# Kernel optimization log

Hardware: AMD Instinct MI355X
Metric: run time of the kernel (lower is better)

## Reference

```python
import jax, jax.numpy as jnp
import numpy as np

EPS = 1e-5  # BatchNorm eps (torch default)
K = 16      # num_neighbors


def _bn(x, gamma, beta, axes):
    # training-mode BatchNorm (biased variance), channel axis = 1
    mu = x.mean(axes, keepdims=True)
    var = x.var(axes, keepdims=True)
    shp = [1] * x.ndim
    shp[1] = -1
    return (x - mu) * jax.lax.rsqrt(var + EPS) * gamma.reshape(shp) + beta.reshape(shp)


def setup_inputs() -> dict:
    key = jax.random.key(0)
    ks = jax.random.split(key, 6)
    B, C, N, E = 4, 3, 4096, 256
    s = lambda k_, shp, fan: jax.random.normal(k_, shp, jnp.float32) * np.float32(1.0 / np.sqrt(fan))
    return {
        "x": jax.random.normal(ks[0], (B, C, N), jnp.float32),
        "g1": jnp.ones((C,), jnp.float32), "b1": jnp.zeros((C,), jnp.float32),
        "W1": s(ks[1], (E, C), C), "bw1": jnp.zeros((E,), jnp.float32),
        "g2a": jnp.ones((C,), jnp.float32), "b2a": jnp.zeros((C,), jnp.float32),
        "W2a": s(ks[2], (E, C), C),
        "g2b": jnp.ones((E,), jnp.float32), "b2b": jnp.zeros((E,), jnp.float32),
        "W2b": s(ks[3], (E, E), E),
        "Wf": s(ks[4], (E, 2 * E), 2 * E), "bf": jnp.zeros((E,), jnp.float32),
    }


def reference(x, g1, b1, W1, bw1, g2a, b2a, W2a, g2b, b2b, W2b, Wf, bf):
    B, C, N = x.shape
    xn = _bn(x, g1, b1, (0, 2))                               # BatchNorm1d
    point_emb = jnp.einsum('ec,bcn->ben', W1, xn) + bw1[None, :, None]  # conv1 (1x1)
    # dist = -||xi - xj||; torch topk(dist, largest=False) picks the K LARGEST
    # distances. Squared distance is monotone in the norm, so top_k on d2 gives
    # identical indices without materializing [B,3,N,N].
    x2 = jnp.sum(xn * xn, axis=1)                             # [B,N]
    d2 = x2[:, :, None] + x2[:, None, :] - 2.0 * jnp.einsum('bcn,bcm->bnm', xn, xn)
    _, idx = jax.lax.top_k(d2, min(K, N))                     # [B,N,K]
    idx = idx[:, :, 1:]                                       # original loop skips index 0
    gathered = jax.vmap(lambda xb, ib: xb[:, ib])(xn, idx)    # [B,C,N,K-1]
    neigh = gathered - xn[:, :, :, None]                      # edge features
    h = _bn(neigh, g2a, b2a, (0, 2, 3))                       # BatchNorm2d(Cin)
    h = jnp.einsum('ec,bcnk->benk', W2a, h)                   # 1x1 conv, no bias
    h = jax.nn.gelu(_bn(h, g2b, b2b, (0, 2, 3)), approximate=False)
    h = jnp.einsum('fe,benk->bfnk', W2b, h)                   # 1x1 conv, no bias
    neigh_emb = h.max(-1)                                     # max over neighbors
    feat = jnp.concatenate([point_emb, neigh_emb], axis=1)    # [B,2E,N]
    return jnp.einsum('of,bfn->bon', Wf, feat) + bf[None, :, None]
```

## Files before the change

kernel.cpp:

```cpp
#include <hip/hip_runtime.h>
#include <float.h>
#include <math.h>

#define EPS 1e-5f
constexpr int B = 4, C = 3, N = 4096, E = 256;
constexpr int KNN = 15;
constexpr int BN_ = B * N;
constexpr int P = 8;
constexpr int SR  = 264;
constexpr int SRF = 520;

typedef short bf8 __attribute__((ext_vector_type(8)));
typedef float f4  __attribute__((ext_vector_type(4)));

static __device__ __forceinline__ unsigned short f2bf(float f) {
    union { float f; unsigned int u; } v; v.f = f;
    unsigned int r = v.u + 0x7FFFu + ((v.u >> 16) & 1u);
    return (unsigned short)(r >> 16);
}
static __device__ __forceinline__ unsigned int pkbf(float a, float b) {
    unsigned int r;
    asm("v_cvt_pk_bf16_f32 %0, %1, %2" : "=v"(r) : "v"(a), "v"(b));
    return r;
}
static __device__ __forceinline__ bf8 ld_bf8(const unsigned short* p) {
    return *(const bf8*)p;
}
static __device__ __forceinline__ float gelu_t(float v) {
    float z = v * fmaf(v * v, 0.07135482f, 1.59576912f);
    float r = __builtin_amdgcn_rcpf(1.f + __expf(z));
    return fmaf(-v, r, v);
}

template <int CTRL>
static __device__ __forceinline__ float dppmax(float x) {
    int xi = __float_as_int(x);
    int yi = __builtin_amdgcn_update_dpp(xi, xi, CTRL, 0xF, 0xF, false);
    return fmaxf(x, __int_as_float(yi));
}
static __device__ __forceinline__ float wave_max_bcast(float x) {
    x = dppmax<0x111>(x);
    x = dppmax<0x112>(x);
    x = dppmax<0x114>(x);
    x = dppmax<0x118>(x);
    x = dppmax<0x142>(x);
    x = dppmax<0x143>(x);
    return __int_as_float(__builtin_amdgcn_readlane(__float_as_int(x), 63));
}

__global__ void bn1_stats(const float* __restrict__ x, float* __restrict__ bn1) {
    int c = blockIdx.x, t = threadIdx.x;
    float s = 0.f, ss = 0.f;
    for (int i4 = t; i4 < BN_ / 4; i4 += 256) {
        int b = i4 >> 10, n4 = i4 & 1023;
        float4 v = ((const float4*)(x + (b * C + c) * N))[n4];
        s += v.x + v.y + v.z + v.w;
        ss += v.x * v.x + v.y * v.y + v.z * v.z + v.w * v.w;
    }
    __shared__ float rs_[256], rss_[256];
    rs_[t] = s; rss_[t] = ss; __syncthreads();
    for (int w = 128; w > 0; w >>= 1) {
        if (t < w) { rs_[t] += rs_[t + w]; rss_[t] += rss_[t + w]; }
        __syncthreads();
    }
    if (t == 0) {
        float mu = rs_[0] / (float)BN_;
        float var = rss_[0] / (float)BN_ - mu * mu;
        bn1[c] = mu; bn1[3 + c] = rsqrtf(var + EPS);
    }
}

__global__ void compute_xn_cvt(const float* __restrict__ x,
                               const float* __restrict__ g1,
                               const float* __restrict__ b1,
                               const float* __restrict__ bn1,
                               float4* __restrict__ xn4,
                               const float* __restrict__ W2b, const float* __restrict__ Wf,
                               unsigned short* __restrict__ w2b_t, unsigned short* __restrict__ wf_t) {
    int blk = blockIdx.x;
    if (blk < BN_ / 256) {
        int i = blk * 256 + threadIdx.x;
        int b = i >> 12, n = i & (N - 1);
        float v[3];
        #pragma unroll
        for (int c = 0; c < C; c++)
            v[c] = (x[(b * C + c) * N + n] - bn1[c]) * bn1[3 + c] * g1[c] + b1[c];
        float4 o; o.x = v[0]; o.y = v[1]; o.z = v[2];
        o.w = v[0] * v[0] + v[1] * v[1] + v[2] * v[2];
        xn4[i] = o;
        return;
    }
    int ch = (blk - BN_ / 256) * 256 + threadIdx.x;
    if (ch < 8192) {
        int lane = ch & 63, kb = (ch >> 6) & 7, ft16 = ch >> 9;
        int row = ft16 * 16 + (lane & 15);
        int col = kb * 32 + (lane >> 4) * 8;
        #pragma unroll
        for (int j = 0; j < 8; j++)
            w2b_t[ch * 8 + j] = f2bf(W2b[row * 256 + col + j]);
    } else {
        int c2 = ch - 8192;
        int lane = c2 & 63, kb = (c2 >> 6) & 15, ot = c2 >> 10;
        int row = ot * 16 + (lane & 15);
        int col = kb * 32 + (lane >> 4) * 8;
        #pragma unroll
        for (int j = 0; j < 8; j++)
            wf_t[c2 * 8 + j] = f2bf(Wf[row * 512 + col + j]);
    }
}

__global__ void __launch_bounds__(256, 4) knn_kernel(const float4* __restrict__ xn4,
                                                     unsigned short* __restrict__ idxout,
                                                     float* __restrict__ S9) {
    __shared__ float smom[4][15][9];
    __shared__ __align__(16) float4 pts[1024];
    int w = threadIdx.x >> 6, lane = threadIdx.x & 63;
    int i = blockIdx.x * 4 + w;
    int b = i >> 12, n = i & (N - 1);
    const float4* xb = xn4 + b * N;
    float4 qv = xb[n];
    float d[64];
    #pragma unroll
    for (int ch = 0; ch < 4; ch++) {
        if (ch) __syncthreads();
        #pragma unroll
        for (int u = 0; u < 4; u++)
            pts[u * 256 + threadIdx.x] = xb[ch * 1024 + u * 256 + threadIdx.x];
        __syncthreads();
        #pragma unroll
        for (int j = 0; j < 16; j++) {
            float4 p = pts[j * 64 + lane];
            d[ch * 16 + j] = qv.w + p.w - 2.f * (qv.x * p.x + qv.y * p.y + qv.z * p.z);
        }
    }
    float cm[8];
    #pragma unroll
    for (int c = 0; c < 8; c++) {
        float v = d[c * 8];
        #pragma unroll
        for (int s = 1; s < 8; s++) v = fmaxf(v, d[c * 8 + s]);
        cm[c] = v;
    }
    float bv = cm[0];
    #pragma unroll
    for (int c = 1; c < 8; c++) bv = fmaxf(bv, cm[c]);

    int myj = 0;
    for (int r = 0; r < 16; r++) {
        float wv = wave_max_bcast(bv);
        unsigned long long msk = __ballot(bv == wv);
        int wl = __ffsll(msk) - 1;
        int gi = 0;
        if (lane == wl) {
            int cstar = 0; bool got = false;
            #pragma unroll
            for (int c = 0; c < 8; c++) {
                bool h = !got && (cm[c] == bv);
                cstar = h ? c : cstar;
                got = got || h;
            }
            int slot = 0;
            #pragma unroll
            for (int c = 0; c < 8; c++) {
                if (c == cstar) {
                    bool g2 = false;
                    #pragma unroll
                    for (int s = 0; s < 8; s++) {
                        bool h = !g2 && (d[c * 8 + s] == bv);
                        slot = h ? (c * 8 + s) : slot;
                        g2 = g2 || h;
                    }
                    #pragma unroll
                    for (int s = 0; s < 8; s++)
                        d[c * 8 + s] = (c * 8 + s == slot) ? -FLT_MAX : d[c * 8 + s];
                    float v = d[c * 8];
                    #pragma unroll
                    for (int s = 1; s < 8; s++) v = fmaxf(v, d[c * 8 + s]);
                    cm[c] = v;
                }
            }
            bv = cm[0];
            #pragma unroll
            for (int c = 1; c < 8; c++) bv = fmaxf(bv, cm[c]);
            gi = slot * 64 + lane;
        }
        int g = __shfl(gi, wl);
        if (lane == r - 1) myj = g;
    }

    bool act = lane < 15;
    if (act) idxout[i * KNN + lane] = (unsigned short)myj;
    float4 pj = xb[act ? myj : n];
    float v0 = pj.x - qv.x, v1 = pj.y - qv.y, v2 = pj.z - qv.z;
    if (act) {
        float* mm = smom[w][lane];
        mm[0] = v0; mm[1] = v1; mm[2] = v2;
        mm[3] = v0 * v0; mm[4] = v1 * v1; mm[5] = v2 * v2;
        mm[6] = v0 * v1; mm[7] = v0 * v2; mm[8] = v1 * v2;
    }
    __syncthreads();
    int t = threadIdx.x;
    if (t < 36) {
        int wsel = t / 9, j = t % 9;
        float a = 0.f;
        #pragma unroll
        for (int u = 0; u < 15; u++) a += smom[wsel][u][j];
        atomicAdd(&S9[((blockIdx.x * 4 + wsel) & 63) * 9 + j], a);
    }
}

__global__ void finalize_stats(const float* __restrict__ S9,
                               const float* __restrict__ g2a, const float* __restrict__ b2a,
                               const float* __restrict__ W2a,
                               const float* __restrict__ g2b, const float* __restrict__ b2b,
                               float* __restrict__ ab, float4* __restrict__ wsb) {
    const float cnt = (float)(BN_ * KNN);
    __shared__ float S[9];
    __shared__ float alpha[3], beta[3], mu[3], Ehh[3][3];
    int t = threadIdx.x;
    if (t < 9) {
        float a = 0.f;
        for (int u = 0; u < 64; u++) a += S9[u * 9 + t];
        S[t] = a;
    }
    __syncthreads();
    if (t == 0) {
        float m[3];
        float s2[3][3];
        s2[0][0] = S[3]; s2[1][1] = S[4]; s2[2][2] = S[5];
        s2[0][1] = s2[1][0] = S[6]; s2[0][2] = s2[2][0] = S[7]; s2[1][2] = s2[2][1] = S[8];
        for (int c = 0; c < 3; c++) {
            m[c] = S[c] / cnt;
            float var = s2[c][c] / cnt - m[c] * m[c];
            alpha[c] = g2a[c] * rsqrtf(var + EPS);
            beta[c]  = b2a[c] - m[c] * alpha[c];
            mu[c] = m[c];
            ab[c] = alpha[c]; ab[3 + c] = beta[c];
        }
        for (int c = 0; c < 3; c++)
            for (int cc = 0; cc < 3; cc++)
                Ehh[c][cc] = alpha[c] * alpha[cc] * (s2[c][cc] / cnt)
                           + alpha[c] * beta[cc] * m[c]
                           + beta[c] * alpha[cc] * m[cc]
                           + beta[c] * beta[cc];
    }
    __syncthreads();
    int e = t;
    float wv[3], Eh[3];
    for (int c = 0; c < 3; c++) { wv[c] = W2a[e * 3 + c]; Eh[c] = alpha[c] * mu[c] + beta[c]; }
    float mean = wv[0] * Eh[0] + wv[1] * Eh[1] + wv[2] * Eh[2];
    float m2 = 0.f;
    for (int c = 0; c < 3; c++)
        for (int cc = 0; cc < 3; cc++) m2 += wv[c] * wv[cc] * Ehh[c][cc];
    float var = m2 - mean * mean;
    float s = g2b[e] * rsqrtf(var + EPS);
    float4 o;
    o.x = wv[0] * s; o.y = wv[1] * s; o.z = wv[2] * s; o.w = b2b[e] - mean * s;
    wsb[e] = o;
}

__global__ void __launch_bounds__(512, 4) fused_final(
        const float4* __restrict__ xn4, const unsigned short* __restrict__ idx,
        const float* __restrict__ ab,
        const float4* __restrict__ wsb,
        const unsigned short* __restrict__ w2b_t,
        const float* __restrict__ W1, const float* __restrict__ bw1,
        const unsigned short* __restrict__ wf_t, const float* __restrict__ bfv,
        float* __restrict__ out) {
    __shared__ __align__(16) unsigned short hh_bf[64 * SR];
    __shared__ __align__(16) unsigned short feat_bf[8 * SRF];
    __shared__ __align__(16) float4 hhat4[P][16];
    int i0 = blockIdx.x * P;
    int t = threadIdx.x;
    int b = i0 >> 12, n0 = i0 & (N - 1);
    const float4* xb = xn4 + b * N;

    if (t < P * KNN) {
        int p = t / KNN, k = t % KNN;
        int j = idx[(i0 + p) * KNN + k];
        float4 pj = xb[j];
        float4 pn = xb[n0 + p];
        float4 h;
        h.x = ab[0] * (pj.x - pn.x) + ab[3];
        h.y = ab[1] * (pj.y - pn.y) + ab[4];
        h.z = ab[2] * (pj.z - pn.z) + ab[5];
        h.w = 0.f;
        hhat4[p][k] = h;
    }
    __syncthreads();

    int w = t >> 6, lane = t & 63;
    int m = lane & 15, q = lane >> 4;

    #pragma unroll 1
    for (int pg = 0; pg < 2; pg++) {
        {
            int ep = t & 127;
            int pq = t >> 7;
            int p  = pg * 4 + pq;
            float4 wA = wsb[2 * ep];
            float4 wB = wsb[2 * ep + 1];
            float g0A = 0.f, g0B = 0.f;
            #pragma unroll
            for (int k = 0; k < KNN; k++) {
                float4 hv = hhat4[p][k];
                float vA = fmaf(wA.x, hv.x, fmaf(wA.y, hv.y, fmaf(wA.z, hv.z, wA.w)));
                float vB = fmaf(wB.x, hv.x, fmaf(wB.y, hv.y, fmaf(wB.z, hv.z, wB.w)));
                float gA = gelu_t(vA), gB = gelu_t(vB);
                *(unsigned int*)&hh_bf[(16 * pq + k) * SR + 2 * ep] = pkbf(gA, gB);
                if (k == 0) { g0A = gA; g0B = gB; }
            }
            *(unsigned int*)&hh_bf[(16 * pq + 15) * SR + 2 * ep] = pkbf(g0A, g0B);
            float4 pv = xb[n0 + p];
            float peA = bw1[2 * ep] + W1[(2 * ep) * 3] * pv.x
                      + W1[(2 * ep) * 3 + 1] * pv.y + W1[(2 * ep) * 3 + 2] * pv.z;
            float peB = bw1[2 * ep + 1] + W1[(2 * ep + 1) * 3] * pv.x
                      + W1[(2 * ep + 1) * 3 + 1] * pv.y + W1[(2 * ep + 1) * 3 + 2] * pv.z;
            *(unsigned int*)&feat_bf[p * SRF + 2 * ep] = pkbf(peA, peB);
        }
        __syncthreads();

        {
            bf8 a0[8], a1[8];
            #pragma unroll
            for (int kb = 0; kb < 8; kb++) {
                a0[kb] = ld_bf8(w2b_t + (w * 2 + 0) * 4096 + kb * 512 + lane * 8);
                a1[kb] = ld_bf8(w2b_t + (w * 2 + 1) * 4096 + kb * 512 + lane * 8);
            }
            #pragma unroll 1
            for (int pp = 0; pp < 4; pp++) {
                bf8 hfr[8];
                #pragma unroll
                for (int kb = 0; kb < 8; kb++)
                    hfr[kb] = ld_bf8(&hh_bf[(16 * pp + m) * SR + kb * 32 + q * 8]);
                f4 acc0 = {0.f, 0.f, 0.f, 0.f};
                f4 acc1 = {0.f, 0.f, 0.f, 0.f};
                #pragma unroll
                for (int kb = 0; kb < 8; kb++) {
                    acc0 = __builtin_amdgcn_mfma_f32_16x16x32_bf16(hfr[kb], a0[kb], acc0, 0, 0, 0);
                    acc1 = __builtin_amdgcn_mfma_f32_16x16x32_bf16(hfr[kb], a1[kb], acc1, 0, 0, 0);
                }
                float mx0 = fmaxf(fmaxf(acc0[0], acc0[1]), fmaxf(acc0[2], acc0[3]));
                float mx1 = fmaxf(fmaxf(acc1[0], acc1[1]), fmaxf(acc1[2], acc1[3]));
                mx0 = fmaxf(mx0, __shfl_xor(mx0, 16));
                mx0 = fmaxf(mx0, __shfl_xor(mx0, 32));
                mx1 = fmaxf(mx1, __shfl_xor(mx1, 16));
                mx1 = fmaxf(mx1, __shfl_xor(mx1, 32));
                if (lane < 16) {
                    feat_bf[(pg * 4 + pp) * SRF + E + (w * 2 + 0) * 16 + lane] = f2bf(mx0);
                    feat_bf[(pg * 4 + pp) * SRF + E + (w * 2 + 1) * 16 + lane] = f2bf(mx1);
                }
            }
        }
        __syncthreads();
    }

    {
        bf8 fb[16];
        #pragma unroll
        for (int kb = 0; kb < 16; kb++)
            fb[kb] = ld_bf8(&feat_bf[(m & 7) * SRF + kb * 32 + q * 8]);
        #pragma unroll
        for (int o2 = 0; o2 < 2; o2++) {
            int ot = w * 2 + o2;
            f4 acc = {0.f, 0.f, 0.f, 0.f};
            #pragma unroll
            for (int kb = 0; kb < 16; kb++) {
                bf8 a = ld_bf8(wf_t + ot * 8192 + kb * 512 + lane * 8);
                acc = __builtin_amdgcn_mfma_f32_16x16x32_bf16(a, fb[kb], acc, 0, 0, 0);
            }
            if (m < P) {
                int o0 = ot * 16 + 4 * q;
                out[(b * E + o0 + 0) * N + n0 + m] = acc[0] + bfv[o0 + 0];
                out[(b * E + o0 + 1) * N + n0 + m] = acc[1] + bfv[o0 + 1];
                out[(b * E + o0 + 2) * N + n0 + m] = acc[2] + bfv[o0 + 2];
                out[(b * E + o0 + 3) * N + n0 + m] = acc[3] + bfv[o0 + 3];
            }
        }
    }
}

extern "C" void kernel_launch(void* const* d_in, const int* in_sizes, int n_in,
                              void* d_out, int out_size, void* d_ws, size_t ws_size,
                              hipStream_t stream) {
    (void)in_sizes; (void)n_in; (void)out_size; (void)ws_size;
    const float* x   = (const float*)d_in[0];
    const float* g1  = (const float*)d_in[1];
    const float* b1  = (const float*)d_in[2];
    const float* W1  = (const float*)d_in[3];
    const float* bw1 = (const float*)d_in[4];
    const float* g2a = (const float*)d_in[5];
    const float* b2a = (const float*)d_in[6];
    const float* W2a = (const float*)d_in[7];
    const float* g2b = (const float*)d_in[8];
    const float* b2b = (const float*)d_in[9];
    const float* W2b = (const float*)d_in[10];
    const float* Wf  = (const float*)d_in[11];
    const float* bfv = (const float*)d_in[12];
    float* out = (float*)d_out;

    char* ws = (char*)d_ws;
    size_t off = 0;
    auto alloc = [&](size_t bytes) { size_t o = off; off = (off + bytes + 255) & ~(size_t)255; return o; };
    float4* xn4           = (float4*)(ws + alloc(sizeof(float4) * BN_));
    unsigned short* idx   = (unsigned short*)(ws + alloc(sizeof(unsigned short) * BN_ * KNN));
    float* bn1            = (float*)(ws + alloc(sizeof(float) * 8));
    float* S9             = (float*)(ws + alloc(sizeof(float) * 64 * 9));
    float* ab             = (float*)(ws + alloc(sizeof(float) * 8));
    float4* wsb           = (float4*)(ws + alloc(sizeof(float4) * E));
    unsigned short* w2bt  = (unsigned short*)(ws + alloc(sizeof(unsigned short) * E * E));
    unsigned short* wft   = (unsigned short*)(ws + alloc(sizeof(unsigned short) * E * 2 * E));

    hipMemsetAsync(S9, 0, sizeof(float) * 64 * 9, stream);

    bn1_stats<<<C, 256, 0, stream>>>(x, bn1);
    compute_xn_cvt<<<BN_ / 256 + (8192 + 16384) / 256, 256, 0, stream>>>(
        x, g1, b1, bn1, xn4, W2b, Wf, w2bt, wft);
    knn_kernel<<<BN_ / 4, 256, 0, stream>>>(xn4, idx, S9);
    finalize_stats<<<1, 256, 0, stream>>>(S9, g2a, b2a, W2a, g2b, b2b, ab, wsb);
    fused_final<<<BN_ / P, 512, 0, stream>>>(xn4, idx, ab, wsb, w2bt, W1, bw1, wft, bfv, out);
}
```

Before: 231.5 us.

## Double-buffer fused_final phases, SoA LDS in knn, fold memset into bn1_stats

fused_final now keeps two hh_bf buffers, so building the GELU activations for point group 1 overlaps with the MFMA pass on group 0, which removes one barrier stage. The launch bound drops from 4 to 2 blocks per CU because the doubled LDS footprint limits occupancy anyway. knn_kernel stores its point tile as four separate float arrays instead of float4, which changes the LDS access pattern. The hipMemsetAsync of S9 is replaced by an extra block in bn1_stats, saving one launch.

```diff
diff --git a/kernel.cpp b/kernel.cpp
--- a/kernel.cpp
+++ b/kernel.cpp
@@ -48,8 +48,13 @@
     return __int_as_float(__builtin_amdgcn_readlane(__float_as_int(x), 63));
 }
 
-__global__ void bn1_stats(const float* __restrict__ x, float* __restrict__ bn1) {
+__global__ void bn1_stats(const float* __restrict__ x, float* __restrict__ bn1,
+                          float* __restrict__ S9) {
     int c = blockIdx.x, t = threadIdx.x;
+    if (c == C) {
+        for (int u = t; u < 64 * 9; u += 256) S9[u] = 0.f;
+        return;
+    }
     float s = 0.f, ss = 0.f;
     for (int i4 = t; i4 < BN_ / 4; i4 += 256) {
         int b = i4 >> 10, n4 = i4 & 1023;
@@ -113,7 +118,7 @@
                                                      unsigned short* __restrict__ idxout,
                                                      float* __restrict__ S9) {
     __shared__ float smom[4][15][9];
-    __shared__ __align__(16) float4 pts[1024];
+    __shared__ float ptx[1024], pty[1024], ptz[1024], ptw[1024];
     int w = threadIdx.x >> 6, lane = threadIdx.x & 63;
     int i = blockIdx.x * 4 + w;
     int b = i >> 12, n = i & (N - 1);
@@ -124,13 +129,17 @@
     for (int ch = 0; ch < 4; ch++) {
         if (ch) __syncthreads();
         #pragma unroll
-        for (int u = 0; u < 4; u++)
-            pts[u * 256 + threadIdx.x] = xb[ch * 1024 + u * 256 + threadIdx.x];
+        for (int u = 0; u < 4; u++) {
+            int s = u * 256 + threadIdx.x;
+            float4 v = xb[ch * 1024 + s];
+            ptx[s] = v.x; pty[s] = v.y; ptz[s] = v.z; ptw[s] = v.w;
+        }
         __syncthreads();
         #pragma unroll
         for (int j = 0; j < 16; j++) {
-            float4 p = pts[j * 64 + lane];
-            d[ch * 16 + j] = qv.w + p.w - 2.f * (qv.x * p.x + qv.y * p.y + qv.z * p.z);
+            int s = j * 64 + lane;
+            d[ch * 16 + j] = qv.w + ptw[s]
+                - 2.f * (qv.x * ptx[s] + qv.y * pty[s] + qv.z * ptz[s]);
         }
     }
     float cm[8];
@@ -259,7 +268,7 @@
     wsb[e] = o;
 }
 
-__global__ void __launch_bounds__(512, 4) fused_final(
+__global__ void __launch_bounds__(512, 2) fused_final(
         const float4* __restrict__ xn4, const unsigned short* __restrict__ idx,
         const float* __restrict__ ab,
         const float4* __restrict__ wsb,
@@ -267,13 +276,74 @@
         const float* __restrict__ W1, const float* __restrict__ bw1,
         const unsigned short* __restrict__ wf_t, const float* __restrict__ bfv,
         float* __restrict__ out) {
-    __shared__ __align__(16) unsigned short hh_bf[64 * SR];
+    __shared__ __align__(16) unsigned short hh_bf[2][64 * SR];
     __shared__ __align__(16) unsigned short feat_bf[8 * SRF];
     __shared__ __align__(16) float4 hhat4[P][16];
     int i0 = blockIdx.x * P;
     int t = threadIdx.x;
     int b = i0 >> 12, n0 = i0 & (N - 1);
     const float4* xb = xn4 + b * N;
+
+    int w = t >> 6, lane = t & 63;
+    int m = lane & 15, q = lane >> 4;
+
+    auto phaseB = [&](int pg) {
+        int ep = t & 127;
+        int pq = t >> 7;
+        int p  = pg * 4 + pq;
+        float4 wA = wsb[2 * ep];
+        float4 wB = wsb[2 * ep + 1];
+        float g0A = 0.f, g0B = 0.f;
+        #pragma unroll
+        for (int k = 0; k < KNN; k++) {
+            float4 hv = hhat4[p][k];
+            float vA = fmaf(wA.x, hv.x, fmaf(wA.y, hv.y, fmaf(wA.z, hv.z, wA.w)));
+            float vB = fmaf(wB.x, hv.x, fmaf(wB.y, hv.y, fmaf(wB.z, hv.z, wB.w)));
+            float gA = gelu_t(vA), gB = gelu_t(vB);
+            *(unsigned int*)&hh_bf[pg][(16 * pq + k) * SR + 2 * ep] = pkbf(gA, gB);
+            if (k == 0) { g0A = gA; g0B = gB; }
+        }
+        *(unsigned int*)&hh_bf[pg][(16 * pq + 15) * SR + 2 * ep] = pkbf(g0A, g0B);
+        float4 pv = xb[n0 + p];
+        float peA = bw1[2 * ep] + W1[(2 * ep) * 3] * pv.x
+                  + W1[(2 * ep) * 3 + 1] * pv.y + W1[(2 * ep) * 3 + 2] * pv.z;
+        float peB = bw1[2 * ep + 1] + W1[(2 * ep + 1) * 3] * pv.x
+                  + W1[(2 * ep + 1) * 3 + 1] * pv.y + W1[(2 * ep + 1) * 3 + 2] * pv.z;
+        *(unsigned int*)&feat_bf[p * SRF + 2 * ep] = pkbf(peA, peB);
+    };
+
+    auto phaseC = [&](int pg) {
+        bf8 a0[8], a1[8];
+        #pragma unroll
+        for (int kb = 0; kb < 8; kb++) {
+            a0[kb] = ld_bf8(w2b_t + (w * 2 + 0) * 4096 + kb * 512 + lane * 8);
+            a1[kb] = ld_bf8(w2b_t + (w * 2 + 1) * 4096 + kb * 512 + lane * 8);
+        }
+        #pragma unroll 1
+        for (int pp = 0; pp < 4; pp++) {
+            bf8 hfr[8];
+            #pragma unroll
+            for (int kb = 0; kb < 8; kb++)
+                hfr[kb] = ld_bf8(&hh_bf[pg][(16 * pp + m) * SR + kb * 32 + q * 8]);
+            f4 acc0 = {0.f, 0.f, 0.f, 0.f};
+            f4 acc1 = {0.f, 0.f, 0.f, 0.f};
+            #pragma unroll
+            for (int kb = 0; kb < 8; kb++) {
+                acc0 = __builtin_amdgcn_mfma_f32_16x16x32_bf16(hfr[kb], a0[kb], acc0, 0, 0, 0);
+                acc1 = __builtin_amdgcn_mfma_f32_16x16x32_bf16(hfr[kb], a1[kb], acc1, 0, 0, 0);
+            }
+            float mx0 = fmaxf(fmaxf(acc0[0], acc0[1]), fmaxf(acc0[2], acc0[3]));
+            float mx1 = fmaxf(fmaxf(acc1[0], acc1[1]), fmaxf(acc1[2], acc1[3]));
+            mx0 = fmaxf(mx0, __shfl_xor(mx0, 16));
+            mx0 = fmaxf(mx0, __shfl_xor(mx0, 32));
+            mx1 = fmaxf(mx1, __shfl_xor(mx1, 16));
+            mx1 = fmaxf(mx1, __shfl_xor(mx1, 32));
+            if (lane < 16) {
+                feat_bf[(pg * 4 + pp) * SRF + E + (w * 2 + 0) * 16 + lane] = f2bf(mx0);
+                feat_bf[(pg * 4 + pp) * SRF + E + (w * 2 + 1) * 16 + lane] = f2bf(mx1);
+            }
+        }
+    };
 
     if (t < P * KNN) {
         int p = t / KNN, k = t % KNN;
@@ -289,71 +359,15 @@
     }
     __syncthreads();
 
-    int w = t >> 6, lane = t & 63;
-    int m = lane & 15, q = lane >> 4;
-
-    #pragma unroll 1
-    for (int pg = 0; pg < 2; pg++) {
-        {
-            int ep = t & 127;
-            int pq = t >> 7;
-            int p  = pg * 4 + pq;
-            float4 wA = wsb[2 * ep];
-            float4 wB = wsb[2 * ep + 1];
-            float g0A = 0.f, g0B = 0.f;
-            #pragma unroll
-            for (int k = 0; k < KNN; k++) {
-                float4 hv = hhat4[p][k];
-                float vA = fmaf(wA.x, hv.x, fmaf(wA.y, hv.y, fmaf(wA.z, hv.z, wA.w)));
-                float vB = fmaf(wB.x, hv.x, fmaf(wB.y, hv.y, fmaf(wB.z, hv.z, wB.w)));
-                float gA = gelu_t(vA), gB = gelu_t(vB);
-                *(unsigned int*)&hh_bf[(16 * pq + k) * SR + 2 * ep] = pkbf(gA, gB);
-                if (k == 0) { g0A = gA; g0B = gB; }
-            }
-            *(unsigned int*)&hh_bf[(16 * pq + 15) * SR + 2 * ep] = pkbf(g0A, g0B);
-            float4 pv = xb[n0 + p];
-            float peA = bw1[2 * ep] + W1[(2 * ep) * 3] * pv.x
-                      + W1[(2 * ep) * 3 + 1] * pv.y + W1[(2 * ep) * 3 + 2] * pv.z;
-            float peB = bw1[2 * ep + 1] + W1[(2 * ep + 1) * 3] * pv.x
-                      + W1[(2 * ep + 1) * 3 + 1] * pv.y + W1[(2 * ep + 1) * 3 + 2] * pv.z;
-            *(unsigned int*)&feat_bf[p * SRF + 2 * ep] = pkbf(peA, peB);
-        }
-        __syncthreads();
-
-        {
-            bf8 a0[8], a1[8];
-            #pragma unroll
-            for (int kb = 0; kb < 8; kb++) {
-                a0[kb] = ld_bf8(w2b_t + (w * 2 + 0) * 4096 + kb * 512 + lane * 8);
-                a1[kb] = ld_bf8(w2b_t + (w * 2 + 1) * 4096 + kb * 512 + lane * 8);
-            }
-            #pragma unroll 1
-            for (int pp = 0; pp < 4; pp++) {
-                bf8 hfr[8];
-                #pragma unroll
-                for (int kb = 0; kb < 8; kb++)
-                    hfr[kb] = ld_bf8(&hh_bf[(16 * pp + m) * SR + kb * 32 + q * 8]);
-                f4 acc0 = {0.f, 0.f, 0.f, 0.f};
-                f4 acc1 = {0.f, 0.f, 0.f, 0.f};
-                #pragma unroll
-                for (int kb = 0; kb < 8; kb++) {
-                    acc0 = __builtin_amdgcn_mfma_f32_16x16x32_bf16(hfr[kb], a0[kb], acc0, 0, 0, 0);
-                    acc1 = __builtin_amdgcn_mfma_f32_16x16x32_bf16(hfr[kb], a1[kb], acc1, 0, 0, 0);
-                }
-                float mx0 = fmaxf(fmaxf(acc0[0], acc0[1]), fmaxf(acc0[2], acc0[3]));
-                float mx1 = fmaxf(fmaxf(acc1[0], acc1[1]), fmaxf(acc1[2], acc1[3]));
-                mx0 = fmaxf(mx0, __shfl_xor(mx0, 16));
-                mx0 = fmaxf(mx0, __shfl_xor(mx0, 32));
-                mx1 = fmaxf(mx1, __shfl_xor(mx1, 16));
-                mx1 = fmaxf(mx1, __shfl_xor(mx1, 32));
-                if (lane < 16) {
-                    feat_bf[(pg * 4 + pp) * SRF + E + (w * 2 + 0) * 16 + lane] = f2bf(mx0);
-                    feat_bf[(pg * 4 + pp) * SRF + E + (w * 2 + 1) * 16 + lane] = f2bf(mx1);
-                }
-            }
-        }
-        __syncthreads();
-    }
+    phaseB(0);
+    __syncthreads();
+
+    phaseB(1);
+    phaseC(0);
+    __syncthreads();
+
+    phaseC(1);
+    __syncthreads();
 
     {
         bf8 fb[16];
@@ -411,9 +425,7 @@
     unsigned short* w2bt  = (unsigned short*)(ws + alloc(sizeof(unsigned short) * E * E));
     unsigned short* wft   = (unsigned short*)(ws + alloc(sizeof(unsigned short) * E * 2 * E));
 
-    hipMemsetAsync(S9, 0, sizeof(float) * 64 * 9, stream);
-
-    bn1_stats<<<C, 256, 0, stream>>>(x, bn1);
+    bn1_stats<<<C + 1, 256, 0, stream>>>(x, bn1, S9);
     compute_xn_cvt<<<BN_ / 256 + (8192 + 16384) / 256, 256, 0, stream>>>(
         x, g1, b1, bn1, xn4, W2b, Wf, w2bt, wft);
     knn_kernel<<<BN_ / 4, 256, 0, stream>>>(xn4, idx, S9);
```

New measurement: 218.1 us. 5.8% less time.
